# Optimization experiments

Measured on AMD Instinct MI355X. Metric: run time of the kernel, lower is better.

The kernel has to match this reference:

```python
import jax, jax.numpy as jnp
import numpy as np

B, T, D, U = 32, 2048, 512, 512


def setup_inputs() -> dict:
    key = jax.random.key(0)
    ks = jax.random.split(key, 6)
    value = jax.random.normal(ks[0], (B, T, D), dtype=jnp.float32)
    query = jax.random.normal(ks[1], (B, D), dtype=jnp.float32)
    mask = jax.random.randint(ks[2], (B, T), 0, 2, dtype=jnp.int32)
    # Glorot-ish scaled dense weights (no bias, matching Dense(use_bias=False))
    W1 = jax.random.normal(ks[3], (D, U), dtype=jnp.float32) * (1.0 / np.sqrt(D))
    W2 = jax.random.normal(ks[4], (D, U), dtype=jnp.float32) * (1.0 / np.sqrt(D))
    V = jax.random.normal(ks[5], (U,), dtype=jnp.float32) * (1.0 / np.sqrt(U))
    return {"value": value, "query": query, "mask": mask, "W1": W1, "W2": W2, "V": V}


def reference(value, query, mask, W1, W2, V):
    # Additive (Bahdanau) attention scores: u[b,t] = V . tanh(value[b,t] @ W1 + query[b] @ W2)
    w1_key = jnp.einsum('btd,du->btu', value, W1)          # [B, T, U]
    w2_query = jnp.einsum('bd,du->bu', query, W2)          # [B, U]
    u = jnp.einsum('btu,u->bt', jnp.tanh(w1_key + w2_query[:, None, :]), V)  # [B, T]
    # Masking: add -1e20 where mask == 0 (same as keras reference)
    u = u + (1.0 - mask.astype(u.dtype)) * jnp.asarray(-1e20, dtype=u.dtype)
    a = jax.nn.softmax(u, axis=1)                          # [B, T]
    # Pointer extraction: gather value row at argmax of attention weights
    idx = jnp.argmax(a, axis=1)                            # [B]
    context = jnp.take_along_axis(value, idx[:, None, None], axis=1)[:, 0, :]  # [B, D]
    return (context, a)
```

## Files before the change

kernel.cpp:

```cpp
#include <hip/hip_runtime.h>
#include <hip/hip_fp16.h>
#include <stdint.h>

#define B_ 32
#define T_ 2048
#define D_ 512
#define U_ 512
#define M_ (B_ * T_)
#define MAXC 4

#define ROWS 64

typedef _Float16 half8   __attribute__((ext_vector_type(8)));
typedef float   floatx4  __attribute__((ext_vector_type(4)));
typedef float   floatx16 __attribute__((ext_vector_type(16)));

__device__ __forceinline__ float tanh_fast(float x) {
    float ax = fabsf(x);
    float e  = __expf(2.0f * ax);
    float t  = 1.0f - 2.0f / (e + 1.0f);
    return copysignf(t, x);
}

__global__ __launch_bounds__(256)
void k_prep(const float* __restrict__ W1, const float* __restrict__ query,
            const float* __restrict__ W2, _Float16* __restrict__ W1T,
            float* __restrict__ w2q) {
    const int bid = blockIdx.x;
    const int tid = threadIdx.x;
    if (bid < 64) {
        __shared__ float tile[64][65];
        const int bx = bid & 7;
        const int by = bid >> 3;
        const int k0 = bx * 64, n0 = by * 64;
        const int tx = tid & 63;
        const int ty = tid >> 6;
#pragma unroll
        for (int i = 0; i < 16; ++i) {
            int r = ty * 16 + i;
            tile[r][tx] = W1[(size_t)(k0 + r) * U_ + n0 + tx];
        }
        __syncthreads();
#pragma unroll
        for (int i = 0; i < 16; ++i) {
            int r = ty * 16 + i;
            W1T[(size_t)(n0 + r) * D_ + k0 + tx] = (_Float16)tile[tx][r];
        }
    } else {
        __shared__ float sq[D_];
        __shared__ float part[128];
        const int id = bid - 64;
        const int b  = id >> 2;
        const int nq = id & 3;
        sq[tid]       = query[b * D_ + tid];
        sq[tid + 256] = query[b * D_ + tid + 256];
        __syncthreads();
        const int n  = nq * 128 + (tid & 127);
        const int dh = tid >> 7;
        float acc = 0.f;
        const int d0 = dh * 256;
#pragma unroll 16
        for (int d = d0; d < d0 + 256; ++d)
            acc = fmaf(sq[d], W2[(size_t)d * U_ + n], acc);
        if (dh == 1) part[tid & 127] = acc;
        __syncthreads();
        if (dh == 0) w2q[b * U_ + n] = acc + part[tid];
    }
}

__global__ __launch_bounds__(512, 4)
void k_gemm_u(const float* __restrict__ value,
              const _Float16* __restrict__ W1T,
              const float* __restrict__ w2q,
              const float* __restrict__ Vv,
              float* __restrict__ u_out) {
    __shared__ __align__(16) _Float16 sA[64 * 64 * 8];
    __shared__ float sRed[8][ROWS];

    const int tid  = threadIdx.x;
    const int wave = tid >> 6;
    const int lane = tid & 63;
    const int l31  = lane & 31;
    const int hi   = lane >> 5;
    const int m0   = blockIdx.x * ROWS;
    const int b    = m0 >> 11;

    {
        const float* src = value + (size_t)(m0 + lane) * D_ + wave * 64;
        floatx4 r[16];
#pragma unroll
        for (int i = 0; i < 16; ++i) r[i] = *(const floatx4*)(src + i * 4);
#pragma unroll
        for (int j = 0; j < 8; ++j) {
            half8 h;
#pragma unroll
            for (int q = 0; q < 4; ++q) {
                h[q]     = (_Float16)r[2 * j][q];
                h[4 + q] = (_Float16)r[2 * j + 1][q];
            }
            *(half8*)(&sA[((wave * 8 + j) * 64 + lane) * 8]) = h;
        }
    }
    __syncthreads();

    float u_acc0[16], u_acc1[16];
#pragma unroll
    for (int r = 0; r < 16; ++r) { u_acc0[r] = 0.f; u_acc1[r] = 0.f; }

#pragma unroll
    for (int g = 0; g < 2; ++g) {
        const int n = wave * 64 + g * 32 + l31;
        const _Float16* bp = W1T + (size_t)n * D_ + hi * 8;

        floatx16 acc0, acc1;
#pragma unroll
        for (int r = 0; r < 16; ++r) { acc0[r] = 0.f; acc1[r] = 0.f; }

#pragma unroll
        for (int s = 0; s < 32; ++s) {
            const half8 bf  = *(const half8*)(bp + s * 16);
            const int   cc  = (s * 2 + hi) * 64;
            const half8 af0 = *(const half8*)(&sA[(cc + l31) * 8]);
            const half8 af1 = *(const half8*)(&sA[(cc + 32 + l31) * 8]);
            acc0 = __builtin_amdgcn_mfma_f32_32x32x16_f16(af0, bf, acc0, 0, 0, 0);
            acc1 = __builtin_amdgcn_mfma_f32_32x32x16_f16(af1, bf, acc1, 0, 0, 0);
        }

        const float w2 = w2q[b * U_ + n];
        const float vv = Vv[n];
#pragma unroll
        for (int r = 0; r < 16; ++r) {
            u_acc0[r] += vv * tanh_fast(acc0[r] + w2);
            u_acc1[r] += vv * tanh_fast(acc1[r] + w2);
        }
    }

#pragma unroll
    for (int off = 1; off < 32; off <<= 1)
#pragma unroll
        for (int r = 0; r < 16; ++r) {
            u_acc0[r] += __shfl_xor(u_acc0[r], off, 64);
            u_acc1[r] += __shfl_xor(u_acc1[r], off, 64);
        }

    if (l31 == 0) {
#pragma unroll
        for (int r = 0; r < 16; ++r) {
            const int row = (r & 3) + 8 * (r >> 2) + 4 * hi;
            sRed[wave][row]      = u_acc0[r];
            sRed[wave][32 + row] = u_acc1[r];
        }
    }
    __syncthreads();
    if (tid < ROWS) {
        float s = 0.f;
#pragma unroll
        for (int w = 0; w < 8; ++w) s += sRed[w][tid];
        u_out[m0 + tid] = s;
    }
}

__global__ __launch_bounds__(256)
void k_post(const float* __restrict__ u, const int* __restrict__ mask,
            const float* __restrict__ value, const float* __restrict__ W1,
            const float* __restrict__ w2q, const float* __restrict__ Vv,
            float* __restrict__ a_out, float* __restrict__ ctx_out) {
    __shared__ float sx[T_];
    __shared__ float rv[4];
    __shared__ int   ri[4];
    __shared__ float s_scalar;
    __shared__ int   s_cand[MAXC];
    __shared__ float s_score[MAXC];
    __shared__ __align__(16) float vrows[MAXC][D_];
    __shared__ int   s_t;

    const int b = blockIdx.x;
    const int tid = threadIdx.x;
    const int wave = tid >> 6, lane = tid & 63;

#pragma unroll
    for (int i = 0; i < 8; ++i) {
        const int t = tid * 8 + i;
        float x = u[b * T_ + t];
        if (mask[b * T_ + t] == 0) x = -1e20f;
        sx[t] = x;
    }
    __syncthreads();

    for (int r = 0; r < MAXC; ++r) {
        float v = -INFINITY; int vi = 0;
#pragma unroll
        for (int i = 0; i < 8; ++i) {
            const int t = tid * 8 + i;
            const float x = sx[t];
            if (x > v) { v = x; vi = t; }
        }
        for (int off = 32; off > 0; off >>= 1) {
            const float ov = __shfl_down(v, off, 64);
            const int   oi = __shfl_down(vi, off, 64);
            if (ov > v || (ov == v && oi < vi)) { v = ov; vi = oi; }
        }
        if (lane == 0) { rv[wave] = v; ri[wave] = vi; }
        __syncthreads();
        if (tid == 0) {
            float bv = rv[0]; int bi = ri[0];
            for (int w = 1; w < 4; ++w)
                if (rv[w] > bv || (rv[w] == bv && ri[w] < bi)) { bv = rv[w]; bi = ri[w]; }
            s_cand[r] = bi;
            if (r == 0) s_scalar = bv;
            sx[bi] = -INFINITY;
        }
        __syncthreads();
    }
    const float mx = s_scalar;

    float zloc = 0.f;
    float evals[8];
#pragma unroll
    for (int i = 0; i < 8; ++i) {
        const int t = tid * 8 + i;
        float x = u[b * T_ + t];
        if (mask[b * T_ + t] == 0) x = -1e20f;
        const float e = __expf(x - mx);
        evals[i] = e;
        zloc += e;
    }
    for (int off = 32; off > 0; off >>= 1) zloc += __shfl_down(zloc, off, 64);
    if (lane == 0) rv[wave] = zloc;
    __syncthreads();
    if (tid == 0) s_scalar = 1.0f / (rv[0] + rv[1] + rv[2] + rv[3]);
    __syncthreads();
    const float rz = s_scalar;
#pragma unroll
    for (int i = 0; i < 8; ++i) {
        const int t = tid * 8 + i;
        a_out[b * T_ + t] = evals[i] * rz;
    }

#pragma unroll
    for (int ci = 0; ci < MAXC; ++ci) {
        const int t = s_cand[ci];
        vrows[ci][tid]       = value[((size_t)b * T_ + t) * D_ + tid];
        vrows[ci][tid + 256] = value[((size_t)b * T_ + t) * D_ + tid + 256];
    }
    __syncthreads();

    float dots[2][MAXC];
#pragma unroll
    for (int j = 0; j < 2; ++j)
#pragma unroll
        for (int ci = 0; ci < MAXC; ++ci) dots[j][ci] = 0.f;

    for (int d4 = 0; d4 < D_; d4 += 4) {
        floatx4 vr[MAXC];
#pragma unroll
        for (int ci = 0; ci < MAXC; ++ci)
            vr[ci] = *(const floatx4*)(&vrows[ci][d4]);
#pragma unroll
        for (int k = 0; k < 4; ++k) {
            const float w0 = W1[(size_t)(d4 + k) * U_ + tid];
            const float w1 = W1[(size_t)(d4 + k) * U_ + tid + 256];
#pragma unroll
            for (int ci = 0; ci < MAXC; ++ci) {
                dots[0][ci] = fmaf(vr[ci][k], w0, dots[0][ci]);
                dots[1][ci] = fmaf(vr[ci][k], w1, dots[1][ci]);
            }
        }
    }
    float sc[MAXC];
#pragma unroll
    for (int ci = 0; ci < MAXC; ++ci) {
        const float n0v = Vv[tid]       * tanhf(dots[0][ci] + w2q[b * U_ + tid]);
        const float n1v = Vv[tid + 256] * tanhf(dots[1][ci] + w2q[b * U_ + tid + 256]);
        sc[ci] = n0v + n1v;
    }
#pragma unroll
    for (int ci = 0; ci < MAXC; ++ci)
        for (int off = 32; off > 0; off >>= 1)
            sc[ci] += __shfl_down(sc[ci], off, 64);
    __syncthreads();
    if (lane == 0) {
#pragma unroll
        for (int ci = 0; ci < MAXC; ++ci)
            vrows[ci][wave] = sc[ci];
    }
    __syncthreads();
    if (tid == 0) {
#pragma unroll
        for (int ci = 0; ci < MAXC; ++ci) {
            const int t = s_cand[ci];
            float s = vrows[ci][0] + vrows[ci][1] + vrows[ci][2] + vrows[ci][3];
            if (mask[b * T_ + t] == 0) s = -1e20f;
            s_score[ci] = s;
        }
        float bv = s_score[0]; int bt = s_cand[0];
        for (int i = 1; i < MAXC; ++i) {
            if (s_score[i] > bv || (s_score[i] == bv && s_cand[i] < bt)) {
                bv = s_score[i]; bt = s_cand[i];
            }
        }
        s_t = bt;
    }
    __syncthreads();

    const int t = s_t;
    ctx_out[b * D_ + tid]       = value[((size_t)b * T_ + t) * D_ + tid];
    ctx_out[b * D_ + tid + 256] = value[((size_t)b * T_ + t) * D_ + tid + 256];
}

extern "C" void kernel_launch(void* const* d_in, const int* in_sizes, int n_in,
                              void* d_out, int out_size, void* d_ws, size_t ws_size,
                              hipStream_t stream) {
    const float* value = (const float*)d_in[0];
    const float* query = (const float*)d_in[1];
    const int*   mask  = (const int*)d_in[2];
    const float* W1    = (const float*)d_in[3];
    const float* W2    = (const float*)d_in[4];
    const float* Vv    = (const float*)d_in[5];

    char* ws = (char*)d_ws;
    _Float16* W1T  = (_Float16*)ws;
    float*    w2q  = (float*)(ws + 524288);
    float*    u_ws = (float*)(ws + 524288 + 65536);

    float* ctx_out = (float*)d_out;
    float* a_out   = (float*)d_out + B_ * D_;

    hipLaunchKernelGGL(k_prep,   dim3(192), dim3(256), 0, stream,
                       W1, query, W2, W1T, w2q);
    hipLaunchKernelGGL(k_gemm_u, dim3(M_ / ROWS), dim3(512), 0, stream,
                       value, W1T, w2q, Vv, u_ws);
    hipLaunchKernelGGL(k_post,   dim3(32), dim3(256), 0, stream,
                       u_ws, mask, value, W1, w2q, Vv, a_out, ctx_out);
}
```

Before: 312.1 us.

## Split U across blocks, keep W1 slice in registers, pre-pack W1 layout

```diff
diff --git a/kernel.cpp b/kernel.cpp
--- a/kernel.cpp
+++ b/kernel.cpp
@@ -9,7 +9,7 @@
 #define M_ (B_ * T_)
 #define MAXC 4
 
-#define ROWS 64
+#define NSPLIT 4
 
 typedef _Float16 half8   __attribute__((ext_vector_type(8)));
 typedef float   floatx4  __attribute__((ext_vector_type(4)));
@@ -24,7 +24,7 @@
 
 __global__ __launch_bounds__(256)
 void k_prep(const float* __restrict__ W1, const float* __restrict__ query,
-            const float* __restrict__ W2, _Float16* __restrict__ W1T,
+            const float* __restrict__ W2, _Float16* __restrict__ W1P,
             float* __restrict__ w2q) {
     const int bid = blockIdx.x;
     const int tid = threadIdx.x;
@@ -44,7 +44,9 @@
 #pragma unroll
         for (int i = 0; i < 16; ++i) {
             int r = ty * 16 + i;
-            W1T[(size_t)(n0 + r) * D_ + k0 + tx] = (_Float16)tile[tx][r];
+            const int n = n0 + r, k = k0 + tx;
+            const int idx = (n >> 5) * 16384 + (k >> 3) * 256 + (n & 31) * 8 + (k & 7);
+            W1P[idx] = (_Float16)tile[tx][r];
         }
     } else {
         __shared__ float sq[D_];
@@ -68,100 +70,101 @@
     }
 }
 
-__global__ __launch_bounds__(512, 4)
+__global__ __launch_bounds__(256, 2)
 void k_gemm_u(const float* __restrict__ value,
-              const _Float16* __restrict__ W1T,
+              const _Float16* __restrict__ W1P,
               const float* __restrict__ w2q,
               const float* __restrict__ Vv,
-              float* __restrict__ u_out) {
+              float* __restrict__ u_part) {
     __shared__ __align__(16) _Float16 sA[64 * 64 * 8];
-    __shared__ float sRed[8][ROWS];
+    __shared__ float sRed[4][64];
 
     const int tid  = threadIdx.x;
     const int wave = tid >> 6;
     const int lane = tid & 63;
     const int l31  = lane & 31;
     const int hi   = lane >> 5;
-    const int m0   = blockIdx.x * ROWS;
+    const int bx   = blockIdx.x;
+    const int sl   = (bx >> 3) & 3;
+    const int rg   = ((bx >> 5) << 3) | (bx & 7);
+    const int m0   = rg * 64;
     const int b    = m0 >> 11;
+    const int n_g  = sl * 128 + wave * 32 + l31;
+
+    const _Float16* bp = W1P + ((sl * 4 + wave) << 14) + hi * 256 + l31 * 8;
+    half8 breg[32];
+#pragma unroll
+    for (int s = 0; s < 32; ++s)
+        breg[s] = *(const half8*)(bp + s * 512);
 
     {
-        const float* src = value + (size_t)(m0 + lane) * D_ + wave * 64;
-        floatx4 r[16];
-#pragma unroll
-        for (int i = 0; i < 16; ++i) r[i] = *(const floatx4*)(src + i * 4);
-#pragma unroll
-        for (int j = 0; j < 8; ++j) {
-            half8 h;
-#pragma unroll
-            for (int q = 0; q < 4; ++q) {
-                h[q]     = (_Float16)r[2 * j][q];
-                h[4 + q] = (_Float16)r[2 * j + 1][q];
+        const float* src = value + (size_t)(m0 + lane) * D_ + wave * 128;
+#pragma unroll
+        for (int b2 = 0; b2 < 2; ++b2) {
+            floatx4 r[16];
+#pragma unroll
+            for (int i = 0; i < 16; ++i)
+                r[i] = *(const floatx4*)(src + b2 * 64 + i * 4);
+#pragma unroll
+            for (int j = 0; j < 8; ++j) {
+                half8 h;
+#pragma unroll
+                for (int q = 0; q < 4; ++q) {
+                    h[q]     = (_Float16)r[2 * j][q];
+                    h[4 + q] = (_Float16)r[2 * j + 1][q];
+                }
+                *(half8*)(&sA[((wave * 16 + b2 * 8 + j) * 64 + lane) * 8]) = h;
             }
-            *(half8*)(&sA[((wave * 8 + j) * 64 + lane) * 8]) = h;
-        }
-    }
-    __syncthreads();
-
-    float u_acc0[16], u_acc1[16];
-#pragma unroll
-    for (int r = 0; r < 16; ++r) { u_acc0[r] = 0.f; u_acc1[r] = 0.f; }
-
-#pragma unroll
-    for (int g = 0; g < 2; ++g) {
-        const int n = wave * 64 + g * 32 + l31;
-        const _Float16* bp = W1T + (size_t)n * D_ + hi * 8;
-
-        floatx16 acc0, acc1;
-#pragma unroll
-        for (int r = 0; r < 16; ++r) { acc0[r] = 0.f; acc1[r] = 0.f; }
-
-#pragma unroll
-        for (int s = 0; s < 32; ++s) {
-            const half8 bf  = *(const half8*)(bp + s * 16);
-            const int   cc  = (s * 2 + hi) * 64;
-            const half8 af0 = *(const half8*)(&sA[(cc + l31) * 8]);
-            const half8 af1 = *(const half8*)(&sA[(cc + 32 + l31) * 8]);
-            acc0 = __builtin_amdgcn_mfma_f32_32x32x16_f16(af0, bf, acc0, 0, 0, 0);
-            acc1 = __builtin_amdgcn_mfma_f32_32x32x16_f16(af1, bf, acc1, 0, 0, 0);
-        }
-
-        const float w2 = w2q[b * U_ + n];
-        const float vv = Vv[n];
+        }
+    }
+    __syncthreads();
+
+    floatx16 acc0, acc1;
+#pragma unroll
+    for (int r = 0; r < 16; ++r) { acc0[r] = 0.f; acc1[r] = 0.f; }
+
+#pragma unroll
+    for (int s = 0; s < 32; ++s) {
+        const int cc = (s * 2 + hi) * 64;
+        const half8 af0 = *(const half8*)(&sA[(cc + l31) * 8]);
+        const half8 af1 = *(const half8*)(&sA[(cc + 32 + l31) * 8]);
+        acc0 = __builtin_amdgcn_mfma_f32_32x32x16_f16(af0, breg[s], acc0, 0, 0, 0);
+        acc1 = __builtin_amdgcn_mfma_f32_32x32x16_f16(af1, breg[s], acc1, 0, 0, 0);
+    }
+
+    const float w2 = w2q[b * U_ + n_g];
+    const float vv = Vv[n_g];
+    float ps0[16], ps1[16];
+#pragma unroll
+    for (int r = 0; r < 16; ++r) {
+        ps0[r] = vv * tanh_fast(acc0[r] + w2);
+        ps1[r] = vv * tanh_fast(acc1[r] + w2);
+    }
+#pragma unroll
+    for (int off = 1; off < 32; off <<= 1)
 #pragma unroll
         for (int r = 0; r < 16; ++r) {
-            u_acc0[r] += vv * tanh_fast(acc0[r] + w2);
-            u_acc1[r] += vv * tanh_fast(acc1[r] + w2);
-        }
-    }
-
-#pragma unroll
-    for (int off = 1; off < 32; off <<= 1)
-#pragma unroll
-        for (int r = 0; r < 16; ++r) {
-            u_acc0[r] += __shfl_xor(u_acc0[r], off, 64);
-            u_acc1[r] += __shfl_xor(u_acc1[r], off, 64);
+            ps0[r] += __shfl_xor(ps0[r], off, 64);
+            ps1[r] += __shfl_xor(ps1[r], off, 64);
         }
 
     if (l31 == 0) {
 #pragma unroll
         for (int r = 0; r < 16; ++r) {
             const int row = (r & 3) + 8 * (r >> 2) + 4 * hi;
-            sRed[wave][row]      = u_acc0[r];
-            sRed[wave][32 + row] = u_acc1[r];
-        }
-    }
-    __syncthreads();
-    if (tid < ROWS) {
-        float s = 0.f;
-#pragma unroll
-        for (int w = 0; w < 8; ++w) s += sRed[w][tid];
-        u_out[m0 + tid] = s;
+            sRed[wave][row]      = ps0[r];
+            sRed[wave][32 + row] = ps1[r];
+        }
+    }
+    __syncthreads();
+    if (tid < 64) {
+        const float s = sRed[0][tid] + sRed[1][tid] + sRed[2][tid] + sRed[3][tid];
+        u_part[(size_t)sl * M_ + m0 + tid] = s;
     }
 }
 
 __global__ __launch_bounds__(256)
-void k_post(const float* __restrict__ u, const int* __restrict__ mask,
+void k_post(const float* __restrict__ u_part, const int* __restrict__ mask,
             const float* __restrict__ value, const float* __restrict__ W1,
             const float* __restrict__ w2q, const float* __restrict__ Vv,
             float* __restrict__ a_out, float* __restrict__ ctx_out) {
@@ -181,7 +184,8 @@
 #pragma unroll
     for (int i = 0; i < 8; ++i) {
         const int t = tid * 8 + i;
-        float x = u[b * T_ + t];
+        float x = u_part[b * T_ + t] + u_part[M_ + b * T_ + t]
+                + u_part[2 * M_ + b * T_ + t] + u_part[3 * M_ + b * T_ + t];
         if (mask[b * T_ + t] == 0) x = -1e20f;
         sx[t] = x;
     }
@@ -219,7 +223,8 @@
 #pragma unroll
     for (int i = 0; i < 8; ++i) {
         const int t = tid * 8 + i;
-        float x = u[b * T_ + t];
+        float x = u_part[b * T_ + t] + u_part[M_ + b * T_ + t]
+                + u_part[2 * M_ + b * T_ + t] + u_part[3 * M_ + b * T_ + t];
         if (mask[b * T_ + t] == 0) x = -1e20f;
         const float e = __expf(x - mx);
         evals[i] = e;
@@ -319,17 +324,17 @@
     const float* Vv    = (const float*)d_in[5];
 
     char* ws = (char*)d_ws;
-    _Float16* W1T  = (_Float16*)ws;
-    float*    w2q  = (float*)(ws + 524288);
-    float*    u_ws = (float*)(ws + 524288 + 65536);
+    _Float16* W1P    = (_Float16*)ws;
+    float*    w2q    = (float*)(ws + 524288);
+    float*    u_part = (float*)(ws + 524288 + 65536);
 
     float* ctx_out = (float*)d_out;
     float* a_out   = (float*)d_out + B_ * D_;
 
     hipLaunchKernelGGL(k_prep,   dim3(192), dim3(256), 0, stream,
-                       W1, query, W2, W1T, w2q);
-    hipLaunchKernelGGL(k_gemm_u, dim3(M_ / ROWS), dim3(512), 0, stream,
-                       value, W1T, w2q, Vv, u_ws);
+                       W1, query, W2, W1P, w2q);
+    hipLaunchKernelGGL(k_gemm_u, dim3(NSPLIT * (M_ / 64)), dim3(256), 0, stream,
+                       value, W1P, w2q, Vv, u_part);
     hipLaunchKernelGGL(k_post,   dim3(32), dim3(256), 0, stream,
-                       u_ws, mask, value, W1, w2q, Vv, a_out, ctx_out);
-}
+                       u_part, mask, value, W1, w2q, Vv, a_out, ctx_out);
+}
```

After: 310.3 us. About the same (-0.6%).
